# Optimization experiments

Hardware: AMD Instinct MI355X
Metric: run time of the kernel (lower is better)

Reference implementation:

```python
import jax, jax.numpy as jnp
import numpy as np

B, N, DIN, HID, DOUT = 1024, 128, 256, 256, 256
KDIM = 4 * N  # fcq/fck output dim = n_node * 4


def setup_inputs() -> dict:
    key = jax.random.key(0)
    ks = jax.random.split(key, 11)
    s = 0.05
    x = jax.random.normal(ks[0], (B, N, DIN), dtype=jnp.float32)
    # binary attention mask in {0,1}
    mask = jax.random.randint(ks[1], (B, N, N), 0, 2).astype(jnp.float32)
    Wv = jax.random.normal(ks[2], (DIN, HID), dtype=jnp.float32) * s
    bv = jax.random.normal(ks[3], (HID,), dtype=jnp.float32) * s
    Wq = jax.random.normal(ks[4], (DIN, KDIM), dtype=jnp.float32) * s
    bq = jax.random.normal(ks[5], (KDIM,), dtype=jnp.float32) * s
    Wk = jax.random.normal(ks[6], (DIN, KDIM), dtype=jnp.float32) * s
    bk = jax.random.normal(ks[7], (KDIM,), dtype=jnp.float32) * s
    Wo = jax.random.normal(ks[8], (HID, DOUT), dtype=jnp.float32) * s
    bo = jax.random.normal(ks[9], (DOUT,), dtype=jnp.float32) * s
    return {"x": x, "mask": mask, "Wv": Wv, "bv": bv, "Wq": Wq, "bq": bq,
            "Wk": Wk, "bk": bk, "Wo": Wo, "bo": bo}


def reference(x, mask, Wv, bv, Wq, bq, Wk, bk, Wo, bo):
    # v: [B,N,HID], q/k: [B,N,4N]
    v = jax.nn.relu(jnp.einsum('bnd,dh->bnh', x, Wv) + bv)
    q = jax.nn.relu(jnp.einsum('bnd,dk->bnk', x, Wq) + bq)
    k = jax.nn.relu(jnp.einsum('bnd,dk->bnk', x, Wk) + bk)
    # scores: bmm(q, k^T) -> [B,N,N]
    scores = jnp.einsum('bnk,bmk->bnm', q, k)
    val = scores * mask - 1000.0 * (1.0 - mask)
    att = jax.nn.softmax(val, axis=2)
    ctx = jnp.einsum('bnm,bmh->bnh', att, v)  # [B,N,HID]
    out = jax.nn.relu(jnp.einsum('bnh,hd->bnd', ctx, Wo) + bo)
    return out, att
```

## Files before the change

### kernel.cpp

```cpp
#include <hip/hip_runtime.h>
#include <cstdint>
#include <cstddef>

#define B_SZ 1024
#define N_SZ 128
#define DIN 256
#define HID 256
#define DOUT 256
#define KD 512

typedef unsigned short u16;
typedef _Float16 f16x8 __attribute__((ext_vector_type(8)));
typedef float floatx4 __attribute__((ext_vector_type(4)));
typedef unsigned short u16x8 __attribute__((ext_vector_type(8)));

#define MFMA16(a,b,c) __builtin_amdgcn_mfma_f32_16x16x32_f16(a, b, c, 0, 0, 0)

__device__ __forceinline__ u16 f2h(float f) {
    _Float16 h = (_Float16)f;
    return *(u16*)&h;
}

__device__ __forceinline__ void gload16(const void* g, void* lds) {
    __builtin_amdgcn_global_load_lds(
        (__attribute__((address_space(1))) void*)const_cast<void*>(g),
        (__attribute__((address_space(3))) void*)lds,
        16, 0, 0);
}

#define XS_OFF  0
#define QS_OFF  65536
#define KS_OFF  81920
#define ATT_OFF 65536
#define WD_OFF  98304
#define RED_OFF 98304

__global__ __launch_bounds__(512, 2)
void fused_att(const float* __restrict__ x,   const float* __restrict__ mask,
               const u16* __restrict__ Wq_t,  const float* __restrict__ bq,
               const u16* __restrict__ Wk_t,  const float* __restrict__ bk,
               const u16* __restrict__ Wv_t,  const float* __restrict__ bv,
               const u16* __restrict__ Wo_t,  const float* __restrict__ bo,
               float* __restrict__ out,       float* __restrict__ att)
{
    __shared__ char LD[131072];

    const int tid  = threadIdx.x;
    const int wid  = tid >> 6;
    const int lane = tid & 63;
    const int l16  = lane & 15;
    const int quad = lane >> 4;
    const int b    = blockIdx.x;

    const int swm = (wid >> 2) * 64;
    const int swn = (wid & 3) * 32;
    const int qm0 = (wid >> 1) * 32;
    const int qn0 = (wid & 1) * 32;

    auto stageQK = [&](const u16* Wqb, const u16* Wkb, int kc, int buf) {
        int row = (wid << 3) + (lane >> 3);
        int g   = (lane & 7) ^ (row & 7);
        char* dst = LD + WD_OFF + buf * 16384 + wid * 1024;
        gload16(Wqb + (size_t)row * DIN + kc * 64 + g * 8, dst);
        gload16(Wkb + (size_t)row * DIN + kc * 64 + g * 8, dst + 8192);
    };
    auto stageW128 = [&](const u16* Wb, int kc, int buf) {
#pragma unroll
        for (int p = 0; p < 2; ++p) {
            int off = p * 8192 + wid * 1024;
            int row = (off >> 7) + (lane >> 3);
            int g   = (lane & 7) ^ (row & 7);
            gload16(Wb + (size_t)row * DIN + kc * 64 + g * 8,
                    LD + WD_OFF + buf * 16384 + off);
        }
    };

    {
        const float* xb = x + (size_t)b * (N_SZ * DIN);
        int row = tid >> 2;
        int c0  = (tid & 3) * 64;
        int sw  = (row & 7) << 4;
        const float* xr = xb + (size_t)row * DIN;
#pragma unroll
        for (int u = 0; u < 8; ++u) {
            int col = c0 + u * 8;
            float4 f0 = *(const float4*)(xr + col);
            float4 f1 = *(const float4*)(xr + col + 4);
            u16x8 o;
            o[0] = f2h(f0.x); o[1] = f2h(f0.y); o[2] = f2h(f0.z); o[3] = f2h(f0.w);
            o[4] = f2h(f1.x); o[5] = f2h(f1.y); o[6] = f2h(f1.z); o[7] = f2h(f1.w);
            *(u16x8*)(LD + ((row * 512 + col * 2) ^ sw)) = o;
        }
    }
    __syncthreads();

    floatx4 sacc[4][2];
#pragma unroll
    for (int i = 0; i < 4; i++)
#pragma unroll
        for (int j = 0; j < 2; j++) sacc[i][j] = floatx4{0.f, 0.f, 0.f, 0.f};

    for (int kd = 0; kd < 8; ++kd) {
        const u16* Wqb = Wq_t + (size_t)(kd * 64) * DIN;
        const u16* Wkb = Wk_t + (size_t)(kd * 64) * DIN;

        floatx4 qa[2][2], ka[2][2];
#pragma unroll
        for (int i = 0; i < 2; i++)
#pragma unroll
            for (int j = 0; j < 2; j++) {
                qa[i][j] = floatx4{0.f, 0.f, 0.f, 0.f};
                ka[i][j] = floatx4{0.f, 0.f, 0.f, 0.f};
            }

        stageQK(Wqb, Wkb, 0, 0);
        __syncthreads();
        for (int kc = 0; kc < 4; ++kc) {
            int buf = kc & 1;
            if (kc < 3) stageQK(Wqb, Wkb, kc + 1, buf ^ 1);
            const char* WQ = LD + WD_OFF + buf * 16384;
            const char* WK = WQ + 8192;
#pragma unroll
            for (int ks = 0; ks < 2; ++ks) {
                f16x8 af[2], qf[2], kf[2];
                int kofs = kc * 64 + ks * 32 + quad * 8;
#pragma unroll
                for (int i = 0; i < 2; ++i) {
                    int r = qm0 + i * 16 + l16;
                    af[i] = *(const f16x8*)(LD + ((r * 512 + kofs * 2) ^ ((r & 7) << 4)));
                }
#pragma unroll
                for (int j = 0; j < 2; ++j) {
                    int n  = qn0 + j * 16 + l16;
                    int by = (n * 128 + (ks * 32 + quad * 8) * 2) ^ ((n & 7) << 4);
                    qf[j] = *(const f16x8*)(WQ + by);
                    kf[j] = *(const f16x8*)(WK + by);
                }
#pragma unroll
                for (int i = 0; i < 2; i++)
#pragma unroll
                    for (int j = 0; j < 2; j++) {
                        qa[i][j] = MFMA16(af[i], qf[j], qa[i][j]);
                        ka[i][j] = MFMA16(af[i], kf[j], ka[i][j]);
                    }
            }
            __syncthreads();
        }

        float bqv[2], bkv[2];
#pragma unroll
        for (int j = 0; j < 2; j++) {
            int col = kd * 64 + qn0 + j * 16 + l16;
            bqv[j] = bq[col];
            bkv[j] = bk[col];
        }
#pragma unroll
        for (int i = 0; i < 2; i++)
#pragma unroll
            for (int j = 0; j < 2; j++)
#pragma unroll
                for (int r = 0; r < 4; r++) {
                    int rw = qm0 + i * 16 + quad * 4 + r;
                    int cl = qn0 + j * 16 + l16;
                    int by = (rw * 128 + cl * 2) ^ ((rw & 7) << 4);
                    *(u16*)(LD + QS_OFF + by) = f2h(fmaxf(qa[i][j][r] + bqv[j], 0.f));
                    *(u16*)(LD + KS_OFF + by) = f2h(fmaxf(ka[i][j][r] + bkv[j], 0.f));
                }
        __syncthreads();

#pragma unroll
        for (int ks = 0; ks < 2; ++ks) {
            f16x8 saf[4], sbf[2];
            int kofs = (ks * 32 + quad * 8) * 2;
#pragma unroll
            for (int i = 0; i < 4; i++) {
                int r = swm + i * 16 + l16;
                saf[i] = *(const f16x8*)(LD + QS_OFF + ((r * 128 + kofs) ^ ((r & 7) << 4)));
            }
#pragma unroll
            for (int j = 0; j < 2; j++) {
                int n = swn + j * 16 + l16;
                sbf[j] = *(const f16x8*)(LD + KS_OFF + ((n * 128 + kofs) ^ ((n & 7) << 4)));
            }
#pragma unroll
            for (int i = 0; i < 4; i++)
#pragma unroll
                for (int j = 0; j < 2; j++)
                    sacc[i][j] = MFMA16(saf[i], sbf[j], sacc[i][j]);
        }
        __syncthreads();
    }

    {
        const float* mb = mask + (size_t)b * (N_SZ * N_SZ);
        float* REDm = (float*)(LD + RED_OFF);
        float* REDs = REDm + 512;
        float rmax[4][4];
#pragma unroll
        for (int i = 0; i < 4; i++) {
#pragma unroll
            for (int r = 0; r < 4; r++) {
                int row = swm + i * 16 + quad * 4 + r;
                float mx = -1e30f;
#pragma unroll
                for (int j = 0; j < 2; j++) {
                    int col = swn + j * 16 + l16;
                    float mval = mb[row * N_SZ + col];
                    float val  = sacc[i][j][r] * mval - 1000.f * (1.f - mval);
                    sacc[i][j][r] = val;
                    mx = fmaxf(mx, val);
                }
#pragma unroll
                for (int s = 1; s < 16; s <<= 1) mx = fmaxf(mx, __shfl_xor(mx, s, 64));
                rmax[i][r] = mx;
            }
        }
        if (l16 == 0) {
#pragma unroll
            for (int i = 0; i < 4; i++)
#pragma unroll
                for (int r = 0; r < 4; r++)
                    REDm[(wid & 3) * 128 + swm + i * 16 + quad * 4 + r] = rmax[i][r];
        }
        __syncthreads();
#pragma unroll
        for (int i = 0; i < 4; i++)
#pragma unroll
            for (int r = 0; r < 4; r++) {
                int row = swm + i * 16 + quad * 4 + r;
                rmax[i][r] = fmaxf(fmaxf(REDm[row], REDm[128 + row]),
                                   fmaxf(REDm[256 + row], REDm[384 + row]));
            }

        float rsum[4][4];
#pragma unroll
        for (int i = 0; i < 4; i++) {
#pragma unroll
            for (int r = 0; r < 4; r++) {
                float s = 0.f;
#pragma unroll
                for (int j = 0; j < 2; j++) {
                    float e = __expf(sacc[i][j][r] - rmax[i][r]);
                    sacc[i][j][r] = e;
                    s += e;
                }
#pragma unroll
                for (int t = 1; t < 16; t <<= 1) s += __shfl_xor(s, t, 64);
                rsum[i][r] = s;
            }
        }
        if (l16 == 0) {
#pragma unroll
            for (int i = 0; i < 4; i++)
#pragma unroll
                for (int r = 0; r < 4; r++)
                    REDs[(wid & 3) * 128 + swm + i * 16 + quad * 4 + r] = rsum[i][r];
        }
        __syncthreads();

        float* ao = att + (size_t)b * (N_SZ * N_SZ);
#pragma unroll
        for (int i = 0; i < 4; i++) {
#pragma unroll
            for (int r = 0; r < 4; r++) {
                int row = swm + i * 16 + quad * 4 + r;
                float inv = 1.f / (REDs[row] + REDs[128 + row] +
                                   REDs[256 + row] + REDs[384 + row]);
#pragma unroll
                for (int j = 0; j < 2; j++) {
                    int col = swn + j * 16 + l16;
                    float a = sacc[i][j][r] * inv;
                    ao[row * N_SZ + col] = a;
                    int by = (row * 256 + col * 2) ^ ((row & 7) << 4);
                    *(u16*)(LD + ATT_OFF + by) = f2h(a);
                }
            }
        }
        __syncthreads();
    }

    floatx4 ctxa[4][4];
#pragma unroll
    for (int i = 0; i < 4; i++)
#pragma unroll
        for (int j = 0; j < 4; j++) ctxa[i][j] = floatx4{0.f, 0.f, 0.f, 0.f};

    for (int hh = 0; hh < 2; ++hh) {
        const u16* Wvb = Wv_t + (size_t)(hh * 128) * DIN;

        floatx4 va[4][2];
#pragma unroll
        for (int i = 0; i < 4; i++)
#pragma unroll
            for (int j = 0; j < 2; j++) va[i][j] = floatx4{0.f, 0.f, 0.f, 0.f};

        stageW128(Wvb, 0, 0);
        __syncthreads();
        for (int kc = 0; kc < 4; ++kc) {
            int buf = kc & 1;
            if (kc < 3) stageW128(Wvb, kc + 1, buf ^ 1);
            const char* WV = LD + WD_OFF + buf * 16384;
#pragma unroll
            for (int ks = 0; ks < 2; ++ks) {
                int kofs = kc * 64 + ks * 32 + quad * 8;
                f16x8 af[4], wf[2];
#pragma unroll
                for (int i = 0; i < 4; i++) {
                    int r = swm + i * 16 + l16;
                    af[i] = *(const f16x8*)(LD + ((r * 512 + kofs * 2) ^ ((r & 7) << 4)));
                }
#pragma unroll
                for (int j = 0; j < 2; j++) {
                    int n = swn + j * 16 + l16;
                    wf[j] = *(const f16x8*)(WV + ((n * 128 + (ks * 32 + quad * 8) * 2) ^ ((n & 7) << 4)));
                }
#pragma unroll
                for (int i = 0; i < 4; i++)
#pragma unroll
                    for (int j = 0; j < 2; j++)
                        va[i][j] = MFMA16(af[i], wf[j], va[i][j]);
            }
            __syncthreads();
        }

        float bvv[2];
#pragma unroll
        for (int j = 0; j < 2; j++) bvv[j] = bv[hh * 128 + swn + j * 16 + l16];
#pragma unroll
        for (int i = 0; i < 4; i++)
#pragma unroll
            for (int j = 0; j < 2; j++)
#pragma unroll
                for (int r = 0; r < 4; r++) {
                    int m = swm + i * 16 + quad * 4 + r;
                    int h = swn + j * 16 + l16;
                    int by = (h * 256 + m * 2) ^ ((h & 7) << 4);
                    *(u16*)(LD + WD_OFF + by) = f2h(fmaxf(va[i][j][r] + bvv[j], 0.f));
                }
        __syncthreads();

#pragma unroll
        for (int ks = 0; ks < 4; ++ks) {
            int kofs = (ks * 32 + quad * 8) * 2;
            f16x8 paf[4], pbf[2];
#pragma unroll
            for (int i = 0; i < 4; i++) {
                int r = swm + i * 16 + l16;
                paf[i] = *(const f16x8*)(LD + ATT_OFF + ((r * 256 + kofs) ^ ((r & 7) << 4)));
            }
#pragma unroll
            for (int j = 0; j < 2; j++) {
                int n = swn + j * 16 + l16;
                pbf[j] = *(const f16x8*)(LD + WD_OFF + ((n * 256 + kofs) ^ ((n & 7) << 4)));
            }
#pragma unroll
            for (int i = 0; i < 4; i++)
#pragma unroll
                for (int j = 0; j < 2; j++)
                    ctxa[i][hh * 2 + j] = MFMA16(paf[i], pbf[j], ctxa[i][hh * 2 + j]);
        }
        __syncthreads();
    }

#pragma unroll
    for (int i = 0; i < 4; i++)
#pragma unroll
        for (int jj = 0; jj < 4; jj++)
#pragma unroll
            for (int r = 0; r < 4; r++) {
                int row = swm + i * 16 + quad * 4 + r;
                int col = (jj >> 1) * 128 + swn + (jj & 1) * 16 + l16;
                int by = (row * 512 + col * 2) ^ ((row & 7) << 4);
                *(u16*)(LD + by) = f2h(ctxa[i][jj][r]);
            }
    __syncthreads();

    float* ob = out + (size_t)b * (N_SZ * DOUT);
    for (int nh = 0; nh < 2; ++nh) {
        const u16* Wob = Wo_t + (size_t)(nh * 128) * HID;

        floatx4 oa[4][2];
#pragma unroll
        for (int i = 0; i < 4; i++)
#pragma unroll
            for (int j = 0; j < 2; j++) oa[i][j] = floatx4{0.f, 0.f, 0.f, 0.f};

        stageW128(Wob, 0, 0);
        __syncthreads();
        for (int kc = 0; kc < 4; ++kc) {
            int buf = kc & 1;
            if (kc < 3) stageW128(Wob, kc + 1, buf ^ 1);
            const char* WO = LD + WD_OFF + buf * 16384;
#pragma unroll
            for (int ks = 0; ks < 2; ++ks) {
                int kofs = kc * 64 + ks * 32 + quad * 8;
                f16x8 caf[4], wof[2];
#pragma unroll
                for (int i = 0; i < 4; i++) {
                    int r = swm + i * 16 + l16;
                    caf[i] = *(const f16x8*)(LD + ((r * 512 + kofs * 2) ^ ((r & 7) << 4)));
                }
#pragma unroll
                for (int j = 0; j < 2; j++) {
                    int n = swn + j * 16 + l16;
                    wof[j] = *(const f16x8*)(WO + ((n * 128 + (ks * 32 + quad * 8) * 2) ^ ((n & 7) << 4)));
                }
#pragma unroll
                for (int i = 0; i < 4; i++)
#pragma unroll
                    for (int j = 0; j < 2; j++)
                        oa[i][j] = MFMA16(caf[i], wof[j], oa[i][j]);
            }
            __syncthreads();
        }

        float bov[2];
#pragma unroll
        for (int j = 0; j < 2; j++) bov[j] = bo[nh * 128 + swn + j * 16 + l16];
#pragma unroll
        for (int i = 0; i < 4; i++)
#pragma unroll
            for (int j = 0; j < 2; j++)
#pragma unroll
                for (int r = 0; r < 4; r++) {
                    int row = swm + i * 16 + quad * 4 + r;
                    int col = nh * 128 + swn + j * 16 + l16;
                    ob[(size_t)row * DOUT + col] = fmaxf(oa[i][j][r] + bov[j], 0.f);
                }
    }
}

__global__ __launch_bounds__(256)
void wtrans(const float* __restrict__ W, u16* __restrict__ Wt, int K, int Nc)
{
    int idx = blockIdx.x * 256 + threadIdx.x;
    if (idx < K * Nc) {
        int k = idx / Nc, n = idx % Nc;
        Wt[(size_t)n * K + k] = f2h(W[idx]);
    }
}

extern "C" void kernel_launch(void* const* d_in, const int* in_sizes, int n_in,
                              void* d_out, int out_size, void* d_ws, size_t ws_size,
                              hipStream_t stream)
{
    const float* x    = (const float*)d_in[0];
    const float* mask = (const float*)d_in[1];
    const float* Wv   = (const float*)d_in[2];
    const float* bv   = (const float*)d_in[3];
    const float* Wq   = (const float*)d_in[4];
    const float* bq   = (const float*)d_in[5];
    const float* Wk   = (const float*)d_in[6];
    const float* bk   = (const float*)d_in[7];
    const float* Wo   = (const float*)d_in[8];
    const float* bo   = (const float*)d_in[9];

    float* out = (float*)d_out;
    float* att = out + (size_t)B_SZ * N_SZ * DOUT;

    char* ws = (char*)d_ws;
    u16* Wq_t = (u16*)ws;
    u16* Wk_t = Wq_t + (size_t)KD * DIN;
    u16* Wv_t = Wk_t + (size_t)KD * DIN;
    u16* Wo_t = Wv_t + (size_t)HID * DIN;

    wtrans<<<(DIN * KD + 255) / 256, 256, 0, stream>>>(Wq, Wq_t, DIN, KD);
    wtrans<<<(DIN * KD + 255) / 256, 256, 0, stream>>>(Wk, Wk_t, DIN, KD);
    wtrans<<<(DIN * HID + 255) / 256, 256, 0, stream>>>(Wv, Wv_t, DIN, HID);
    wtrans<<<(HID * DOUT + 255) / 256, 256, 0, stream>>>(Wo, Wo_t, HID, DOUT);

    fused_att<<<B_SZ, 512, 0, stream>>>(x, mask,
                                        Wq_t, bq, Wk_t, bk, Wv_t, bv, Wo_t, bo,
                                        out, att);

    (void)in_sizes; (void)n_in; (void)out_size; (void)ws_size;
}
```

Measured before the change: 520.5 us.

## Register-staged weight prefetch pipeline with custom barriers and merged V/O passes

```diff
diff --git a/kernel.cpp b/kernel.cpp
--- a/kernel.cpp
+++ b/kernel.cpp
@@ -21,11 +21,15 @@
     return *(u16*)&h;
 }
 
-__device__ __forceinline__ void gload16(const void* g, void* lds) {
-    __builtin_amdgcn_global_load_lds(
-        (__attribute__((address_space(1))) void*)const_cast<void*>(g),
-        (__attribute__((address_space(3))) void*)lds,
-        16, 0, 0);
+__device__ __forceinline__ void barx() {
+    asm volatile("" ::: "memory");
+    __builtin_amdgcn_s_barrier();
+    asm volatile("" ::: "memory");
+}
+__device__ __forceinline__ void bar_lgkm() {
+    asm volatile("s_waitcnt lgkmcnt(0)" ::: "memory");
+    __builtin_amdgcn_s_barrier();
+    asm volatile("" ::: "memory");
 }
 
 #define XS_OFF  0
@@ -57,23 +61,33 @@
     const int qm0 = (wid >> 1) * 32;
     const int qn0 = (wid & 1) * 32;
 
-    auto stageQK = [&](const u16* Wqb, const u16* Wkb, int kc, int buf) {
-        int row = (wid << 3) + (lane >> 3);
-        int g   = (lane & 7) ^ (row & 7);
-        char* dst = LD + WD_OFF + buf * 16384 + wid * 1024;
-        gload16(Wqb + (size_t)row * DIN + kc * 64 + g * 8, dst);
-        gload16(Wkb + (size_t)row * DIN + kc * 64 + g * 8, dst + 8192);
+    const int srow  = tid >> 3;
+    const int sg    = tid & 7;
+    const int swz16 = (sg * 16) ^ ((srow & 7) << 4);
+
+    auto waddr = [&](const u16* Wb, int ch) -> const u16x8* {
+        int kdv = ch >> 2, kcv = ch & 3;
+        return (const u16x8*)(Wb + ((size_t)(kdv * 64) + srow) * DIN + kcv * 64 + sg * 8);
     };
-    auto stageW128 = [&](const u16* Wb, int kc, int buf) {
-#pragma unroll
-        for (int p = 0; p < 2; ++p) {
-            int off = p * 8192 + wid * 1024;
-            int row = (off >> 7) + (lane >> 3);
-            int g   = (lane & 7) ^ (row & 7);
-            gload16(Wb + (size_t)row * DIN + kc * 64 + g * 8,
-                    LD + WD_OFF + buf * 16384 + off);
-        }
+    auto stage_writeQK = [&](int buf, u16x8 q8, u16x8 k8) {
+        char* base = LD + WD_OFF + buf * 16384 + srow * 128 + swz16;
+        *(u16x8*)base          = q8;
+        *(u16x8*)(base + 8192) = k8;
     };
+    auto load256 = [&](const u16* Wb, int kc, u16x8* r4) {
+#pragma unroll
+        for (int p = 0; p < 4; ++p)
+            r4[p] = *(const u16x8*)(Wb + (size_t)(p * 64 + srow) * DIN + kc * 64 + sg * 8);
+    };
+    auto stage_write256 = [&](const u16x8* r4) {
+#pragma unroll
+        for (int p = 0; p < 4; ++p)
+            *(u16x8*)(LD + WD_OFF + (p * 64 + srow) * 128 + swz16) = r4[p];
+    };
+
+    u16x8 rq[2], rk[2];
+    rq[0] = *waddr(Wq_t, 0); rk[0] = *waddr(Wk_t, 0);
+    rq[1] = *waddr(Wq_t, 1); rk[1] = *waddr(Wk_t, 1);
 
     {
         const float* xb = x + (size_t)b * (N_SZ * DIN);
@@ -92,7 +106,18 @@
             *(u16x8*)(LD + ((row * 512 + col * 2) ^ sw)) = o;
         }
     }
-    __syncthreads();
+    stage_writeQK(0, rq[0], rk[0]);
+    bar_lgkm();
+
+    f16x8 xa[2][8];
+#pragma unroll
+    for (int i = 0; i < 2; ++i)
+#pragma unroll
+        for (int t = 0; t < 8; ++t) {
+            int r = qm0 + i * 16 + l16;
+            int kofs = t * 32 + quad * 8;
+            xa[i][t] = *(const f16x8*)(LD + ((r * 512 + kofs * 2) ^ ((r & 7) << 4)));
+        }
 
     floatx4 sacc[4][2];
 #pragma unroll
@@ -101,52 +126,6 @@
         for (int j = 0; j < 2; j++) sacc[i][j] = floatx4{0.f, 0.f, 0.f, 0.f};
 
     for (int kd = 0; kd < 8; ++kd) {
-        const u16* Wqb = Wq_t + (size_t)(kd * 64) * DIN;
-        const u16* Wkb = Wk_t + (size_t)(kd * 64) * DIN;
-
-        floatx4 qa[2][2], ka[2][2];
-#pragma unroll
-        for (int i = 0; i < 2; i++)
-#pragma unroll
-            for (int j = 0; j < 2; j++) {
-                qa[i][j] = floatx4{0.f, 0.f, 0.f, 0.f};
-                ka[i][j] = floatx4{0.f, 0.f, 0.f, 0.f};
-            }
-
-        stageQK(Wqb, Wkb, 0, 0);
-        __syncthreads();
-        for (int kc = 0; kc < 4; ++kc) {
-            int buf = kc & 1;
-            if (kc < 3) stageQK(Wqb, Wkb, kc + 1, buf ^ 1);
-            const char* WQ = LD + WD_OFF + buf * 16384;
-            const char* WK = WQ + 8192;
-#pragma unroll
-            for (int ks = 0; ks < 2; ++ks) {
-                f16x8 af[2], qf[2], kf[2];
-                int kofs = kc * 64 + ks * 32 + quad * 8;
-#pragma unroll
-                for (int i = 0; i < 2; ++i) {
-                    int r = qm0 + i * 16 + l16;
-                    af[i] = *(const f16x8*)(LD + ((r * 512 + kofs * 2) ^ ((r & 7) << 4)));
-                }
-#pragma unroll
-                for (int j = 0; j < 2; ++j) {
-                    int n  = qn0 + j * 16 + l16;
-                    int by = (n * 128 + (ks * 32 + quad * 8) * 2) ^ ((n & 7) << 4);
-                    qf[j] = *(const f16x8*)(WQ + by);
-                    kf[j] = *(const f16x8*)(WK + by);
-                }
-#pragma unroll
-                for (int i = 0; i < 2; i++)
-#pragma unroll
-                    for (int j = 0; j < 2; j++) {
-                        qa[i][j] = MFMA16(af[i], qf[j], qa[i][j]);
-                        ka[i][j] = MFMA16(af[i], kf[j], ka[i][j]);
-                    }
-            }
-            __syncthreads();
-        }
-
         float bqv[2], bkv[2];
 #pragma unroll
         for (int j = 0; j < 2; j++) {
@@ -154,33 +133,77 @@
             bqv[j] = bq[col];
             bkv[j] = bk[col];
         }
+        floatx4 qa[2][2], ka[2][2];
 #pragma unroll
         for (int i = 0; i < 2; i++)
 #pragma unroll
+            for (int j = 0; j < 2; j++) {
+                qa[i][j] = floatx4{0.f, 0.f, 0.f, 0.f};
+                ka[i][j] = floatx4{0.f, 0.f, 0.f, 0.f};
+            }
+
+#pragma unroll
+        for (int kc = 0; kc < 4; ++kc) {
+            const int ch  = kd * 4 + kc;
+            const int par = kc & 1;
+            if (ch + 2 < 32) {
+                rq[par] = *waddr(Wq_t, ch + 2);
+                rk[par] = *waddr(Wk_t, ch + 2);
+            }
+            const char* WQ = LD + WD_OFF + par * 16384;
+            const char* WK = WQ + 8192;
+            __builtin_amdgcn_s_setprio(1);
+#pragma unroll
+            for (int ks = 0; ks < 2; ++ks) {
+                f16x8 qf[2], kf[2];
+#pragma unroll
+                for (int j = 0; j < 2; ++j) {
+                    int n  = qn0 + j * 16 + l16;
+                    int by = (n * 128) + (((ks * 32 + quad * 8) * 2) ^ ((n & 7) << 4));
+                    qf[j] = *(const f16x8*)(WQ + by);
+                    kf[j] = *(const f16x8*)(WK + by);
+                }
+#pragma unroll
+                for (int i = 0; i < 2; i++)
+#pragma unroll
+                    for (int j = 0; j < 2; j++) {
+                        qa[i][j] = MFMA16(xa[i][kc * 2 + ks], qf[j], qa[i][j]);
+                        ka[i][j] = MFMA16(xa[i][kc * 2 + ks], kf[j], ka[i][j]);
+                    }
+            }
+            __builtin_amdgcn_s_setprio(0);
+            if (ch + 1 < 32) stage_writeQK(par ^ 1, rq[par ^ 1], rk[par ^ 1]);
+            bar_lgkm();
+        }
+
+#pragma unroll
+        for (int i = 0; i < 2; i++)
+#pragma unroll
             for (int j = 0; j < 2; j++)
 #pragma unroll
                 for (int r = 0; r < 4; r++) {
-                    int rw = qm0 + i * 16 + quad * 4 + r;
-                    int cl = qn0 + j * 16 + l16;
-                    int by = (rw * 128 + cl * 2) ^ ((rw & 7) << 4);
+                    int rw_ = qm0 + i * 16 + quad * 4 + r;
+                    int cl  = qn0 + j * 16 + l16;
+                    int by  = (rw_ * 128) + ((cl * 2) ^ ((rw_ & 7) << 4));
                     *(u16*)(LD + QS_OFF + by) = f2h(fmaxf(qa[i][j][r] + bqv[j], 0.f));
                     *(u16*)(LD + KS_OFF + by) = f2h(fmaxf(ka[i][j][r] + bkv[j], 0.f));
                 }
-        __syncthreads();
-
+        bar_lgkm();
+
+        __builtin_amdgcn_s_setprio(1);
 #pragma unroll
         for (int ks = 0; ks < 2; ++ks) {
             f16x8 saf[4], sbf[2];
-            int kofs = (ks * 32 + quad * 8) * 2;
+            int kb2 = (ks * 32 + quad * 8) * 2;
 #pragma unroll
             for (int i = 0; i < 4; i++) {
                 int r = swm + i * 16 + l16;
-                saf[i] = *(const f16x8*)(LD + QS_OFF + ((r * 128 + kofs) ^ ((r & 7) << 4)));
+                saf[i] = *(const f16x8*)(LD + QS_OFF + (r * 128) + (kb2 ^ ((r & 7) << 4)));
             }
 #pragma unroll
             for (int j = 0; j < 2; j++) {
                 int n = swn + j * 16 + l16;
-                sbf[j] = *(const f16x8*)(LD + KS_OFF + ((n * 128 + kofs) ^ ((n & 7) << 4)));
+                sbf[j] = *(const f16x8*)(LD + KS_OFF + (n * 128) + (kb2 ^ ((n & 7) << 4)));
             }
 #pragma unroll
             for (int i = 0; i < 4; i++)
@@ -188,11 +211,24 @@
                 for (int j = 0; j < 2; j++)
                     sacc[i][j] = MFMA16(saf[i], sbf[j], sacc[i][j]);
         }
-        __syncthreads();
+        __builtin_amdgcn_s_setprio(0);
     }
 
+    u16x8 rw[4];
+    load256(Wv_t, 0, rw);
     {
         const float* mb = mask + (size_t)b * (N_SZ * N_SZ);
+        float mreg[4][4][2];
+#pragma unroll
+        for (int i = 0; i < 4; i++)
+#pragma unroll
+            for (int r = 0; r < 4; r++) {
+                int row = swm + i * 16 + quad * 4 + r;
+#pragma unroll
+                for (int j = 0; j < 2; j++)
+                    mreg[i][r][j] = mb[row * N_SZ + swn + j * 16 + l16];
+            }
+
         float* REDm = (float*)(LD + RED_OFF);
         float* REDs = REDm + 512;
         float rmax[4][4];
@@ -200,12 +236,10 @@
         for (int i = 0; i < 4; i++) {
 #pragma unroll
             for (int r = 0; r < 4; r++) {
-                int row = swm + i * 16 + quad * 4 + r;
                 float mx = -1e30f;
 #pragma unroll
                 for (int j = 0; j < 2; j++) {
-                    int col = swn + j * 16 + l16;
-                    float mval = mb[row * N_SZ + col];
+                    float mval = mreg[i][r][j];
                     float val  = sacc[i][j][r] * mval - 1000.f * (1.f - mval);
                     sacc[i][j][r] = val;
                     mx = fmaxf(mx, val);
@@ -222,7 +256,7 @@
                 for (int r = 0; r < 4; r++)
                     REDm[(wid & 3) * 128 + swm + i * 16 + quad * 4 + r] = rmax[i][r];
         }
-        __syncthreads();
+        bar_lgkm();
 #pragma unroll
         for (int i = 0; i < 4; i++)
 #pragma unroll
@@ -256,7 +290,7 @@
                 for (int r = 0; r < 4; r++)
                     REDs[(wid & 3) * 128 + swm + i * 16 + quad * 4 + r] = rsum[i][r];
         }
-        __syncthreads();
+        bar_lgkm();
 
         float* ao = att + (size_t)b * (N_SZ * N_SZ);
 #pragma unroll
@@ -271,12 +305,12 @@
                     int col = swn + j * 16 + l16;
                     float a = sacc[i][j][r] * inv;
                     ao[row * N_SZ + col] = a;
-                    int by = (row * 256 + col * 2) ^ ((row & 7) << 4);
+                    int by = (row * 256) + ((col * 2) ^ ((row & 7) << 4));
                     *(u16*)(LD + ATT_OFF + by) = f2h(a);
                 }
             }
         }
-        __syncthreads();
+        bar_lgkm();
     }
 
     floatx4 ctxa[4][4];
@@ -285,81 +319,85 @@
 #pragma unroll
         for (int j = 0; j < 4; j++) ctxa[i][j] = floatx4{0.f, 0.f, 0.f, 0.f};
 
-    for (int hh = 0; hh < 2; ++hh) {
-        const u16* Wvb = Wv_t + (size_t)(hh * 128) * DIN;
-
-        floatx4 va[4][2];
+    {
+        floatx4 va[4][4];
 #pragma unroll
         for (int i = 0; i < 4; i++)
 #pragma unroll
-            for (int j = 0; j < 2; j++) va[i][j] = floatx4{0.f, 0.f, 0.f, 0.f};
-
-        stageW128(Wvb, 0, 0);
-        __syncthreads();
+            for (int j = 0; j < 4; j++) va[i][j] = floatx4{0.f, 0.f, 0.f, 0.f};
+
+#pragma unroll
         for (int kc = 0; kc < 4; ++kc) {
-            int buf = kc & 1;
-            if (kc < 3) stageW128(Wvb, kc + 1, buf ^ 1);
-            const char* WV = LD + WD_OFF + buf * 16384;
+            stage_write256(rw);
+            if (kc < 3) load256(Wv_t, kc + 1, rw);
+            else        load256(Wo_t, 0, rw);
+            bar_lgkm();
+            __builtin_amdgcn_s_setprio(1);
 #pragma unroll
             for (int ks = 0; ks < 2; ++ks) {
                 int kofs = kc * 64 + ks * 32 + quad * 8;
-                f16x8 af[4], wf[2];
+                f16x8 af[4], wf[4];
 #pragma unroll
                 for (int i = 0; i < 4; i++) {
                     int r = swm + i * 16 + l16;
                     af[i] = *(const f16x8*)(LD + ((r * 512 + kofs * 2) ^ ((r & 7) << 4)));
                 }
 #pragma unroll
-                for (int j = 0; j < 2; j++) {
-                    int n = swn + j * 16 + l16;
-                    wf[j] = *(const f16x8*)(WV + ((n * 128 + (ks * 32 + quad * 8) * 2) ^ ((n & 7) << 4)));
+                for (int jj = 0; jj < 4; jj++) {
+                    int n = (jj >> 1) * 128 + swn + (jj & 1) * 16 + l16;
+                    wf[jj] = *(const f16x8*)(LD + WD_OFF + (n * 128) +
+                                             (((ks * 32 + quad * 8) * 2) ^ ((n & 7) << 4)));
                 }
 #pragma unroll
                 for (int i = 0; i < 4; i++)
 #pragma unroll
-                    for (int j = 0; j < 2; j++)
-                        va[i][j] = MFMA16(af[i], wf[j], va[i][j]);
-            }
-            __syncthreads();
-        }
-
-        float bvv[2];
-#pragma unroll
-        for (int j = 0; j < 2; j++) bvv[j] = bv[hh * 128 + swn + j * 16 + l16];
+                    for (int jj = 0; jj < 4; jj++)
+                        va[i][jj] = MFMA16(af[i], wf[jj], va[i][jj]);
+            }
+            __builtin_amdgcn_s_setprio(0);
+            barx();
+        }
+
+        float bvv[4];
+#pragma unroll
+        for (int jj = 0; jj < 4; jj++)
+            bvv[jj] = bv[(jj >> 1) * 128 + swn + (jj & 1) * 16 + l16];
 #pragma unroll
         for (int i = 0; i < 4; i++)
 #pragma unroll
-            for (int j = 0; j < 2; j++)
+            for (int jj = 0; jj < 4; jj++)
 #pragma unroll
                 for (int r = 0; r < 4; r++) {
                     int m = swm + i * 16 + quad * 4 + r;
-                    int h = swn + j * 16 + l16;
-                    int by = (h * 256 + m * 2) ^ ((h & 7) << 4);
-                    *(u16*)(LD + WD_OFF + by) = f2h(fmaxf(va[i][j][r] + bvv[j], 0.f));
-                }
-        __syncthreads();
-
+                    int h = (jj >> 1) * 128 + swn + (jj & 1) * 16 + l16;
+                    int by = (h * 256) + ((m * 2) ^ ((h & 7) << 4));
+                    *(u16*)(LD + by) = f2h(fmaxf(va[i][jj][r] + bvv[jj], 0.f));
+                }
+        bar_lgkm();
+
+        __builtin_amdgcn_s_setprio(1);
 #pragma unroll
         for (int ks = 0; ks < 4; ++ks) {
-            int kofs = (ks * 32 + quad * 8) * 2;
-            f16x8 paf[4], pbf[2];
+            int kb2 = (ks * 32 + quad * 8) * 2;
+            f16x8 paf[4], pbf[4];
 #pragma unroll
             for (int i = 0; i < 4; i++) {
                 int r = swm + i * 16 + l16;
-                paf[i] = *(const f16x8*)(LD + ATT_OFF + ((r * 256 + kofs) ^ ((r & 7) << 4)));
-            }
-#pragma unroll
-            for (int j = 0; j < 2; j++) {
-                int n = swn + j * 16 + l16;
-                pbf[j] = *(const f16x8*)(LD + WD_OFF + ((n * 256 + kofs) ^ ((n & 7) << 4)));
+                paf[i] = *(const f16x8*)(LD + ATT_OFF + (r * 256) + (kb2 ^ ((r & 7) << 4)));
+            }
+#pragma unroll
+            for (int jj = 0; jj < 4; jj++) {
+                int h = (jj >> 1) * 128 + swn + (jj & 1) * 16 + l16;
+                pbf[jj] = *(const f16x8*)(LD + (h * 256) + (kb2 ^ ((h & 7) << 4)));
             }
 #pragma unroll
             for (int i = 0; i < 4; i++)
 #pragma unroll
-                for (int j = 0; j < 2; j++)
-                    ctxa[i][hh * 2 + j] = MFMA16(paf[i], pbf[j], ctxa[i][hh * 2 + j]);
-        }
-        __syncthreads();
+                for (int jj = 0; jj < 4; jj++)
+                    ctxa[i][jj] = MFMA16(paf[i], pbf[jj], ctxa[i][jj]);
+        }
+        __builtin_amdgcn_s_setprio(0);
+        barx();
     }
 
 #pragma unroll
@@ -370,62 +408,63 @@
             for (int r = 0; r < 4; r++) {
                 int row = swm + i * 16 + quad * 4 + r;
                 int col = (jj >> 1) * 128 + swn + (jj & 1) * 16 + l16;
-                int by = (row * 512 + col * 2) ^ ((row & 7) << 4);
+                int by  = (row * 512) + ((col * 2) ^ ((row & 7) << 4));
                 *(u16*)(LD + by) = f2h(ctxa[i][jj][r]);
             }
-    __syncthreads();
-
-    float* ob = out + (size_t)b * (N_SZ * DOUT);
-    for (int nh = 0; nh < 2; ++nh) {
-        const u16* Wob = Wo_t + (size_t)(nh * 128) * HID;
-
-        floatx4 oa[4][2];
+    bar_lgkm();
+
+    {
+        floatx4 oa[4][4];
 #pragma unroll
         for (int i = 0; i < 4; i++)
 #pragma unroll
-            for (int j = 0; j < 2; j++) oa[i][j] = floatx4{0.f, 0.f, 0.f, 0.f};
-
-        stageW128(Wob, 0, 0);
-        __syncthreads();
+            for (int j = 0; j < 4; j++) oa[i][j] = floatx4{0.f, 0.f, 0.f, 0.f};
+
+#pragma unroll
         for (int kc = 0; kc < 4; ++kc) {
-            int buf = kc & 1;
-            if (kc < 3) stageW128(Wob, kc + 1, buf ^ 1);
-            const char* WO = LD + WD_OFF + buf * 16384;
+            stage_write256(rw);
+            if (kc < 3) load256(Wo_t, kc + 1, rw);
+            bar_lgkm();
+            __builtin_amdgcn_s_setprio(1);
 #pragma unroll
             for (int ks = 0; ks < 2; ++ks) {
                 int kofs = kc * 64 + ks * 32 + quad * 8;
-                f16x8 caf[4], wof[2];
+                f16x8 caf[4], wof[4];
 #pragma unroll
                 for (int i = 0; i < 4; i++) {
                     int r = swm + i * 16 + l16;
                     caf[i] = *(const f16x8*)(LD + ((r * 512 + kofs * 2) ^ ((r & 7) << 4)));
                 }
 #pragma unroll
-                for (int j = 0; j < 2; j++) {
-                    int n = swn + j * 16 + l16;
-                    wof[j] = *(const f16x8*)(WO + ((n * 128 + (ks * 32 + quad * 8) * 2) ^ ((n & 7) << 4)));
+                for (int jj = 0; jj < 4; jj++) {
+                    int n = (jj >> 1) * 128 + swn + (jj & 1) * 16 + l16;
+                    wof[jj] = *(const f16x8*)(LD + WD_OFF + (n * 128) +
+                                              (((ks * 32 + quad * 8) * 2) ^ ((n & 7) << 4)));
                 }
 #pragma unroll
                 for (int i = 0; i < 4; i++)
 #pragma unroll
-                    for (int j = 0; j < 2; j++)
-                        oa[i][j] = MFMA16(caf[i], wof[j], oa[i][j]);
-            }
-            __syncthreads();
-        }
-
-        float bov[2];
-#pragma unroll
-        for (int j = 0; j < 2; j++) bov[j] = bo[nh * 128 + swn + j * 16 + l16];
+                    for (int jj = 0; jj < 4; jj++)
+                        oa[i][jj] = MFMA16(caf[i], wof[jj], oa[i][jj]);
+            }
+            __builtin_amdgcn_s_setprio(0);
+            if (kc < 3) barx();
+        }
+
+        float* ob = out + (size_t)b * (N_SZ * DOUT);
+        float bov[4];
+#pragma unroll
+        for (int jj = 0; jj < 4; jj++)
+            bov[jj] = bo[(jj >> 1) * 128 + swn + (jj & 1) * 16 + l16];
 #pragma unroll
         for (int i = 0; i < 4; i++)
 #pragma unroll
-            for (int j = 0; j < 2; j++)
+            for (int jj = 0; jj < 4; jj++)
 #pragma unroll
                 for (int r = 0; r < 4; r++) {
                     int row = swm + i * 16 + quad * 4 + r;
-                    int col = nh * 128 + swn + j * 16 + l16;
-                    ob[(size_t)row * DOUT + col] = fmaxf(oa[i][j][r] + bov[j], 0.f);
+                    int col = (jj >> 1) * 128 + swn + (jj & 1) * 16 + l16;
+                    ob[(size_t)row * DOUT + col] = fmaxf(oa[i][jj][r] + bov[jj], 0.f);
                 }
     }
 }
```

Measured after the change: 475.2 us. -8.7%, faster.
